# Performance work log

Hardware: AMD Instinct MI355X
Metric: run time of the kernel (lower is better)

## Reference

```python
import jax, jax.numpy as jnp
import numpy as np
from jax import lax

NEG = -1e30  # log-space 'zero' that stays finite for stable grads


def _logadd3(a, b, c):
    m = jnp.maximum(jnp.maximum(a, b), c)
    return m + jnp.log(jnp.exp(a - m) + jnp.exp(b - m) + jnp.exp(c - m))


def _logadd2(a, b):
    m = jnp.maximum(a, b)
    return m + jnp.log(jnp.exp(a - m) + jnp.exp(b - m))


def setup_inputs() -> dict:
    key = jax.random.key(0)
    k1, k2, k3 = jax.random.split(key, 3)
    B, T, V, L = 64, 2000, 512, 200
    logits = jax.random.normal(k1, (B, T, V), dtype=jnp.float32)
    # keep input lengths well above 2*L+1 so all paths are feasible
    input_lengths = (T - jax.random.randint(k2, (B,), 0, 256)).astype(jnp.int32)
    targets = jax.random.randint(k3, (B, L), 0, V, dtype=jnp.int32)  # 0 == pad == blank
    return {"logits": logits, "input_lengths": input_lengths, "targets": targets}


def ctc_loss_sum(logits, input_lengths, targets):
    B, T, V = logits.shape
    L = targets.shape[1]
    S = 2 * L + 1

    lp = jax.nn.log_softmax(logits, axis=-1)  # [B,T,V]

    # compact nonzero targets per row (masked_select equivalent, fixed shape)
    mask = targets != 0
    tlen = mask.sum(-1)  # [B] target_lengths
    pos = jnp.where(mask, jnp.cumsum(mask, axis=1) - 1, L)
    compact = jnp.zeros_like(targets).at[jnp.arange(B)[:, None], pos].set(targets, mode="drop")

    # extended label sequence: blank, y1, blank, y2, ..., blank  -> [B,S]
    s_idx = jnp.arange(S)
    lab_idx = jnp.clip((s_idx - 1) // 2, 0, L - 1)
    ext = jnp.where(s_idx % 2 == 1, compact[:, lab_idx], 0)  # [B,S]

    # skip transition s-2 -> s allowed iff label at s is non-blank and differs from s-2
    ext_m2 = jnp.pad(ext, ((0, 0), (2, 0)))[:, :S]
    skip_ok = (ext != 0) & (ext != ext_m2) & (s_idx >= 2)  # [B,S]

    lpT = jnp.transpose(lp, (1, 0, 2))  # [T,B,V], scan over time

    # init: alpha_0[0]=lp(blank), alpha_0[1]=lp(y1)
    lp0_ext = jnp.take_along_axis(lpT[0], ext[:, :2], axis=1)  # [B,2]
    alpha0 = jnp.full((B, S), NEG, dtype=lp.dtype).at[:, :2].set(lp0_ext)

    def step(alpha, inp):
        lp_t, t = inp
        a1 = jnp.pad(alpha, ((0, 0), (1, 0)), constant_values=NEG)[:, :S]
        a2 = jnp.pad(alpha, ((0, 0), (2, 0)), constant_values=NEG)[:, :S]
        a2 = jnp.where(skip_ok, a2, NEG)
        lp_e = jnp.take_along_axis(lp_t, ext, axis=1)  # [B,S]
        new = _logadd3(alpha, a1, a2) + lp_e
        active = (t < input_lengths)[:, None]
        return jnp.where(active, new, alpha), None

    alphaT, _ = lax.scan(step, alpha0, (lpT[1:], jnp.arange(1, T)))

    # read out at final blank (2*tlen) and final label (2*tlen-1)
    e1 = (2 * tlen)[:, None]
    e2 = (2 * tlen - 1)
    a1 = jnp.take_along_axis(alphaT, e1, axis=1)[:, 0]
    a2 = jnp.where(e2 >= 0,
                   jnp.take_along_axis(alphaT, jnp.clip(e2, 0)[:, None], axis=1)[:, 0],
                   NEG)
    ll = _logadd2(a1, a2)  # [B] log p(targets | logits)
    return -jnp.sum(ll)


def reference(logits, input_lengths, targets):
    return ctc_loss_sum(logits, input_lengths, targets)
```

## Files before the change

### kernel.cpp

```cpp
#include <hip/hip_runtime.h>

#define B_ 64
#define T_ 2000
#define V_ 512
#define L_ 200
#define CPR 7


__device__ __forceinline__ float dpp_shr1_f(float x) {
  return __int_as_float(__builtin_amdgcn_update_dpp(0, __float_as_int(x), 0x138, 0xf, 0xf, true));
}
__device__ __forceinline__ int dpp_shr1_i(int x) {
  return __builtin_amdgcn_update_dpp(0, x, 0x138, 0xf, 0xf, true);
}
__device__ __forceinline__ float dpp_shl1_f(float x) {
  return __int_as_float(__builtin_amdgcn_update_dpp(0, __float_as_int(x), 0x130, 0xf, 0xf, true));
}
__device__ __forceinline__ int dpp_shl1_i(int x) {
  return __builtin_amdgcn_update_dpp(0, x, 0x130, 0xf, 0xf, true);
}
#define DPPADD(v, ctrl, rmask)                                                              \
  v += __int_as_float(__builtin_amdgcn_update_dpp(0, __float_as_int(v), ctrl, rmask, 0xf, true));

__global__ void kz(float* __restrict__ out) { out[0] = 0.0f; }

__global__ __launch_bounds__(512, 1) void ctc_fused(const float* __restrict__ logits,
                                                    const int* __restrict__ lens,
                                                    const int* __restrict__ targets,
                                                    float* __restrict__ AF,
                                                    int* __restrict__ EF,
                                                    float* __restrict__ DD,
                                                    int* __restrict__ EB) {
  const int bx = blockIdx.x;
  const int b = bx >> 1;
  const int dirb = bx & 1;
  const int wid = threadIdx.x >> 6;
  const int lane = threadIdx.x & 63;

  __shared__ __align__(16) float ring[2][CPR][8][256];
  __shared__ __align__(16) float ringbl[2][CPR][8];
  __shared__ __align__(16) float scr[CPR][2][512];
  __shared__ int cmp[256];
  __shared__ int tl_s;

  if (wid == 0) {
    cmp[lane] = 0; cmp[64 + lane] = 0; cmp[128 + lane] = 0; cmp[192 + lane] = 0;
    int base = 0;
#pragma unroll
    for (int cc = 0; cc < 4; ++cc) {
      const int l = cc * 64 + lane;
      const int v = (l < L_) ? targets[b * L_ + l] : 0;
      const unsigned long long mk = __ballot(v != 0);
      const int pos = base + __popcll(mk & ((1ull << lane) - 1ull));
      if (v != 0) cmp[pos] = v;
      base += __popcll(mk);
    }
    if (lane == 0) tl_s = base;
  }
  __syncthreads();

  const int len = lens[b];
  const int nfull = len >> 3;
  const int rem = len & 7;
  const int nch = nfull + (rem ? 1 : 0);
  const int Cf = nch >> 1;
  const int Ntot = dirb ? (nch - Cf) : Cf;
  const int R = (Ntot + CPR - 1) / CPR;
  const int4 c4 = *(const int4*)(&cmp[4 * lane]);

  const int l0 = 4 * lane;
  const bool v0 = l0 + 0 < L_, v1 = l0 + 1 < L_, v2 = l0 + 2 < L_, v3 = l0 + 3 < L_;

  float a0 = 0.f, a1 = 0.f, a2 = 0.f, a3 = 0.f, a4 = 0.f, a5 = 0.f, a6 = 0.f, a7 = 0.f;
  int E = 0;
  float fac = 1.0f;
  float m0 = 0.f, m1 = 0.f, m2 = 0.f, m3 = 0.f, m0n = 0.f;
  float4 LQ0[8], LQ1[8];
  float4 BLa0, BLb0, BLa1, BLb1;

  if (wid == CPR) {
    const int cm1 = __shfl_up(c4.w, 1);
    m0 = (lane > 0 && c4.x != 0 && c4.x != cm1) ? 1.0f : 0.0f;
    m1 = (c4.y != 0 && c4.y != c4.x) ? 1.0f : 0.0f;
    m2 = (c4.z != 0 && c4.z != c4.y) ? 1.0f : 0.0f;
    m3 = (c4.w != 0 && c4.w != c4.z) ? 1.0f : 0.0f;
    m0n = dpp_shl1_f(m0);
    if (!dirb) {
      if (lane == 0) a0 = 1.0f;
    } else {
      const int st = 2 * tl_s;
      if (lane == (st >> 3)) {
        const int e = st & 7;
        a0 = (e == 0) ? 1.0f : 0.0f; a1 = (e == 1) ? 1.0f : 0.0f;
        a2 = (e == 2) ? 1.0f : 0.0f; a3 = (e == 3) ? 1.0f : 0.0f;
        a4 = (e == 4) ? 1.0f : 0.0f; a5 = (e == 5) ? 1.0f : 0.0f;
        a6 = (e == 6) ? 1.0f : 0.0f; a7 = (e == 7) ? 1.0f : 0.0f;
      }
    }
    __builtin_amdgcn_s_setprio(1);
  }

  auto produce = [&](int c, int buf) {
    const float* rowp = logits + (size_t)b * (T_ * V_) + (size_t)c * (8 * V_);
    float4 X[16];
#pragma unroll
    for (int r = 0; r < 8; ++r) {
      X[2 * r] = *(const float4*)(rowp + r * V_ + 4 * lane);
      X[2 * r + 1] = *(const float4*)(rowp + r * V_ + 256 + 4 * lane);
    }
#pragma unroll
    for (int r = 0; r < 8; ++r) {
      const float4 xe = X[2 * r], xo = X[2 * r + 1];
      const float e0 = __expf(xe.x), e1 = __expf(xe.y), e2 = __expf(xe.z), e3 = __expf(xe.w);
      const float e4 = __expf(xo.x), e5 = __expf(xo.y), e6 = __expf(xo.z), e7 = __expf(xo.w);
      float s = ((e0 + e1) + (e2 + e3)) + ((e4 + e5) + (e6 + e7));
      DPPADD(s, 0x111, 0xf); DPPADD(s, 0x112, 0xf); DPPADD(s, 0x114, 0xf);
      DPPADD(s, 0x118, 0xf); DPPADD(s, 0x142, 0xa); DPPADD(s, 0x143, 0xc);
      const float sum = __int_as_float(__builtin_amdgcn_readlane(__float_as_int(s), 63));
      const float inv = 32.0f / sum;
      float* sc = &scr[wid][r & 1][0];
      *(float4*)(sc + 4 * lane) = make_float4(e0, e1, e2, e3);
      *(float4*)(sc + 256 + 4 * lane) = make_float4(e4, e5, e6, e7);
      asm volatile("s_waitcnt lgkmcnt(0)" ::: "memory");
      float4 h;
      h.x = v0 ? sc[c4.x] * inv : 0.0f;
      h.y = v1 ? sc[c4.y] * inv : 0.0f;
      h.z = v2 ? sc[c4.z] * inv : 0.0f;
      h.w = v3 ? sc[c4.w] * inv : 0.0f;
      *(float4*)(&ring[buf][wid][r][4 * lane]) = h;
      if (lane == 0) ringbl[buf][wid][r] = e0 * inv;
    }
  };

#define LDCHUNK(S, BUF, K)                                                   \
  {                                                                          \
    const int bf_ = (BUF), kk_ = (K);                                        \
    _Pragma("unroll") for (int u = 0; u < 8; ++u)                            \
        LQ##S[u] = *(const float4*)(&ring[bf_][kk_][u][4 * lane]);           \
    BLa##S = *(const float4*)(&ringbl[bf_][kk_][0]);                         \
    BLb##S = *(const float4*)(&ringbl[bf_][kk_][4]);                         \
  }

#define STEP8F(S)                                                            \
  {                                                                          \
    const float blv_[8] = {BLa##S.x, BLa##S.y, BLa##S.z, BLa##S.w,           \
                           BLb##S.x, BLb##S.y, BLb##S.z, BLb##S.w};          \
    _Pragma("unroll") for (int u = 0; u < 8; ++u) {                          \
      const float4 hq = LQ##S[u];                                            \
      const float pbv = blv_[u];                                             \
      const float s1 = dpp_shr1_f(a7) * fac;                 \
      float n0 = (a0 + s1) * pbv;                                            \
      float n1 = fmaf(m0, s1, a0 + a1) * hq.x;                               \
      float n2 = (a2 + a1) * pbv;                                            \
      float n3 = fmaf(m1, a1, a2 + a3) * hq.y;                               \
      float n4 = (a4 + a3) * pbv;                                            \
      float n5 = fmaf(m2, a3, a4 + a5) * hq.z;                               \
      float n6 = (a6 + a5) * pbv;                                            \
      float n7 = fmaf(m3, a5, a6 + a7) * hq.w;                               \
      a0 = n0; a1 = n1; a2 = n2; a3 = n3;                                    \
      a4 = n4; a5 = n5; a6 = n6; a7 = n7;                                    \
    }                                                                        \
  }

#define STEP8B(S, UHI)                                                       \
  {                                                                          \
    const float blv_[8] = {BLa##S.x, BLa##S.y, BLa##S.z, BLa##S.w,           \
                           BLb##S.x, BLb##S.y, BLb##S.z, BLb##S.w};          \
    _Pragma("unroll") for (int u = 7; u >= 0; --u) {                         \
      if (u <= (UHI)) {                                                      \
        const float4 hq = LQ##S[u];                                          \
        const float pbv = blv_[u];                                           \
        const float sa = dpp_shl1_f(a0) * fac;              \
        const float sb = dpp_shl1_f(a1) * fac;                               \
        float n0 = (a0 + a1) * pbv;                                          \
        float n1 = fmaf(m1, a3, a1 + a2) * hq.x;                             \
        float n2 = (a2 + a3) * pbv;                                          \
        float n3 = fmaf(m2, a5, a3 + a4) * hq.y;                             \
        float n4 = (a4 + a5) * pbv;                                          \
        float n5 = fmaf(m3, a7, a5 + a6) * hq.z;                             \
        float n6 = (a6 + a7) * pbv;                                          \
        float n7 = fmaf(m0n, sb, a7 + sa) * hq.w;                            \
        a0 = n0; a1 = n1; a2 = n2; a3 = n3;                                  \
        a4 = n4; a5 = n5; a6 = n6; a7 = n7;                                  \
      }                                                                      \
    }                                                                        \
  }

#define RENORM_COMMON                                                        \
    const float mx = fmaxf(fmaxf(fmaxf(a0, a1), fmaxf(a2, a3)),              \
                           fmaxf(fmaxf(a4, a5), fmaxf(a6, a7)));             \
    const bool dead = (mx == 0.0f);                                          \
    int e_ = (int)((__float_as_uint(mx) >> 23) & 0xff) - 127;                \
    if (dead) e_ = 0;                                                        \
    const float sc_ = __int_as_float((unsigned)(127 - e_) << 23);            \
    a0 *= sc_; a1 *= sc_; a2 *= sc_; a3 *= sc_;                              \
    a4 *= sc_; a5 *= sc_; a6 *= sc_; a7 *= sc_;                              \
    const int En_ = E + e_;

#define RENORMF                                                              \
  {                                                                          \
    RENORM_COMMON                                                            \
    const int EnP_ = dpp_shr1_i(En_);                                        \
    E = dead ? EnP_ : En_;                                                   \
    const int Ep_ = dpp_shr1_i(E);                                           \
    const int d_ = Ep_ - E;                                                  \
    int dc_ = d_ < -126 ? -126 : (d_ > 126 ? 126 : d_);                      \
    fac = (d_ < -126) ? 0.0f : __int_as_float((unsigned)(dc_ + 127) << 23);  \
  }

#define RENORMB                                                              \
  {                                                                          \
    RENORM_COMMON                                                            \
    const int EnP_ = dpp_shl1_i(En_);                                        \
    E = dead ? EnP_ : En_;                                                   \
    const int Ep_ = dpp_shl1_i(E);                                           \
    const int d_ = Ep_ - E;                                                  \
    int dc_ = d_ < -126 ? -126 : (d_ > 126 ? 126 : d_);                      \
    fac = (d_ < -126) ? 0.0f : __int_as_float((unsigned)(dc_ + 127) << 23);  \
  }

  if (wid < CPR) {
    const int j = wid;
    if (j < Ntot) produce(dirb ? (nch - 1 - j) : j, 0);
  }
  __syncthreads();

  for (int r = 0; r < R; ++r) {
    if (wid < CPR) {
      const int j = (r + 1) * CPR + wid;
      if (r + 1 < R && j < Ntot) produce(dirb ? (nch - 1 - j) : j, (r + 1) & 1);
    } else {
      int kn = Ntot - r * CPR;
      if (kn > CPR) kn = CPR;
      LDCHUNK(0, r & 1, 0);
      if (!dirb) {
        for (int k = 0; k < kn; ++k) {
          if (k & 1) {
            if (k + 1 < kn) LDCHUNK(0, r & 1, k + 1);
            STEP8F(1);
          } else {
            if (k + 1 < kn) LDCHUNK(1, r & 1, k + 1);
            STEP8F(0);
          }
          RENORMF;
        }
      } else {
        for (int k = 0; k < kn; ++k) {
          const int uh = (r == 0 && k == 0 && rem) ? (rem - 1) : 7;
          if (k & 1) {
            if (k + 1 < kn) LDCHUNK(0, r & 1, k + 1);
            STEP8B(1, uh);
          } else {
            if (k + 1 < kn) LDCHUNK(1, r & 1, k + 1);
            STEP8B(0, uh);
          }
          RENORMB;
        }
      }
    }
    __syncthreads();
  }

  if (wid == CPR) {
    if (!dirb) {
      *(float4*)(AF + b * 512 + lane * 8) = make_float4(a0, a1, a2, a3);
      *(float4*)(AF + b * 512 + lane * 8 + 4) = make_float4(a4, a5, a6, a7);
      EF[b * 64 + lane] = E;
    } else {
      const float sa = dpp_shl1_f(a0) * fac;
      const float sb = dpp_shl1_f(a1) * fac;
      const float d0 = a0 + a1;
      const float d1 = fmaf(m1, a3, a1 + a2);
      const float d2 = a2 + a3;
      const float d3 = fmaf(m2, a5, a3 + a4);
      const float d4 = a4 + a5;
      const float d5 = fmaf(m3, a7, a5 + a6);
      const float d6 = a6 + a7;
      const float d7 = fmaf(m0n, sb, a7 + sa);
      *(float4*)(DD + b * 512 + lane * 8) = make_float4(d0, d1, d2, d3);
      *(float4*)(DD + b * 512 + lane * 8 + 4) = make_float4(d4, d5, d6, d7);
      EB[b * 64 + lane] = E;
    }
  }
#undef LDCHUNK
#undef STEP8F
#undef STEP8B
#undef RENORM_COMMON
#undef RENORMF
#undef RENORMB
}

__global__ __launch_bounds__(64) void kcomb(const int* __restrict__ lens,
                                            const float* __restrict__ AF,
                                            const int* __restrict__ EF,
                                            const float* __restrict__ DD,
                                            const int* __restrict__ EB,
                                            float* __restrict__ out) {
  const int b = blockIdx.x;
  const int lane = threadIdx.x;
  const float4 f0 = *(const float4*)(AF + b * 512 + lane * 8);
  const float4 f1 = *(const float4*)(AF + b * 512 + lane * 8 + 4);
  const float4 g0 = *(const float4*)(DD + b * 512 + lane * 8);
  const float4 g1 = *(const float4*)(DD + b * 512 + lane * 8 + 4);
  const float dot = ((f0.x * g0.x + f0.y * g0.y) + (f0.z * g0.z + f0.w * g0.w)) +
                    ((f1.x * g1.x + f1.y * g1.y) + (f1.z * g1.z + f1.w * g1.w));
  const int Es = EF[b * 64 + lane] + EB[b * 64 + lane];
  const bool z = (dot == 0.0f);
  int Ek = z ? (-(1 << 28)) : Es;
#pragma unroll
  for (int off = 32; off; off >>= 1) {
    const int o = __shfl_xor(Ek, off);
    Ek = o > Ek ? o : Ek;
  }
  float v = z ? 0.0f : ldexpf(dot, Es - Ek);
#pragma unroll
  for (int off = 32; off; off >>= 1) v += __shfl_xor(v, off);
  if (lane == 0) {
    const float ll = __logf(v) + (float)Ek * 0.69314718056f - (float)lens[b] * 3.46573590280f;
    atomicAdd(out, -ll);
  }
}

extern "C" void kernel_launch(void* const* d_in, const int* in_sizes, int n_in,
                              void* d_out, int out_size, void* d_ws, size_t ws_size,
                              hipStream_t stream) {
  const float* logits = (const float*)d_in[0];
  const int* input_lengths = (const int*)d_in[1];
  const int* targets = (const int*)d_in[2];
  float* out = (float*)d_out;
  float* AF = (float*)d_ws;
  int* EF = (int*)(AF + B_ * 512);
  float* DD = (float*)(EF + B_ * 64);
  int* EB = (int*)(DD + B_ * 512);
  (void)in_sizes; (void)n_in; (void)out_size; (void)ws_size;

  kz<<<1, 1, 0, stream>>>(out);
  ctc_fused<<<2 * B_, 512, 0, stream>>>(logits, input_lengths, targets, AF, EF, DD, EB);
  kcomb<<<B_, 64, 0, stream>>>(input_lengths, AF, EF, DD, EB, out);
}
```

Baseline: 396.1 us.

## Split CTC into producer blocks and flag-polling recurrence consumer blocks

Replaces the per-batch 512-thread block, where 7 producer waves fed one recurrence wave through an LDS ring, with a grid of independent 64-thread producer blocks. Each producer block computes the softmax-gathered label probabilities for one 8-frame chunk, stores them to global memory as fp16, and raises a per-chunk flag. 128 consumer blocks run the forward/backward recurrences, polling those flags and prefetching four chunks ahead. The aim is to spread softmax work across the whole GPU instead of capping it at 7 waves per sequence. In exchange it relies on the consumer blocks being scheduled before or alongside the producers, since low-numbered consumers spin-wait and could deadlock otherwise. It also reduces precision to fp16 for label probabilities and replaces the atomic final sum with a single-block reduction.

```diff
diff --git a/kernel.cpp b/kernel.cpp
--- a/kernel.cpp
+++ b/kernel.cpp
@@ -4,8 +4,12 @@
 #define T_ 2000
 #define V_ 512
 #define L_ 200
-#define CPR 7
-
+#define NCONS 128
+#define NPRODB (B_ * 250)
+
+
+typedef _Float16 half4 __attribute__((ext_vector_type(4)));
+union H4U { unsigned long long u; half4 h; float2 f2; };
 
 __device__ __forceinline__ float dpp_shr1_f(float x) {
   return __int_as_float(__builtin_amdgcn_update_dpp(0, __float_as_int(x), 0x138, 0xf, 0xf, true));
@@ -22,85 +26,50 @@
 #define DPPADD(v, ctrl, rmask)                                                              \
   v += __int_as_float(__builtin_amdgcn_update_dpp(0, __float_as_int(v), ctrl, rmask, 0xf, true));
 
-__global__ void kz(float* __restrict__ out) { out[0] = 0.0f; }
-
-__global__ __launch_bounds__(512, 1) void ctc_fused(const float* __restrict__ logits,
-                                                    const int* __restrict__ lens,
-                                                    const int* __restrict__ targets,
-                                                    float* __restrict__ AF,
-                                                    int* __restrict__ EF,
-                                                    float* __restrict__ DD,
-                                                    int* __restrict__ EB) {
-  const int bx = blockIdx.x;
-  const int b = bx >> 1;
-  const int dirb = bx & 1;
-  const int wid = threadIdx.x >> 6;
-  const int lane = threadIdx.x & 63;
-
-  __shared__ __align__(16) float ring[2][CPR][8][256];
-  __shared__ __align__(16) float ringbl[2][CPR][8];
-  __shared__ __align__(16) float scr[CPR][2][512];
+__global__ __launch_bounds__(64) void kflags(int* __restrict__ flags) {
+  const int base = blockIdx.x * 256 + threadIdx.x;
+  flags[base] = 0; flags[base + 64] = 0; flags[base + 128] = 0; flags[base + 192] = 0;
+}
+
+__global__ __launch_bounds__(64, 8) void ctc_split(
+    const float* __restrict__ logits, const int* __restrict__ lens,
+    const int* __restrict__ targets, unsigned long long* __restrict__ cull,
+    unsigned long long* __restrict__ bull, int* __restrict__ flags,
+    float* __restrict__ AF, int* __restrict__ EF,
+    float* __restrict__ DD, int* __restrict__ EB) {
+  const int lane = threadIdx.x;
   __shared__ int cmp[256];
-  __shared__ int tl_s;
-
-  if (wid == 0) {
-    cmp[lane] = 0; cmp[64 + lane] = 0; cmp[128 + lane] = 0; cmp[192 + lane] = 0;
-    int base = 0;
-#pragma unroll
-    for (int cc = 0; cc < 4; ++cc) {
-      const int l = cc * 64 + lane;
-      const int v = (l < L_) ? targets[b * L_ + l] : 0;
-      const unsigned long long mk = __ballot(v != 0);
-      const int pos = base + __popcll(mk & ((1ull << lane) - 1ull));
-      if (v != 0) cmp[pos] = v;
-      base += __popcll(mk);
-    }
-    if (lane == 0) tl_s = base;
-  }
-  __syncthreads();
-
-  const int len = lens[b];
-  const int nfull = len >> 3;
-  const int rem = len & 7;
-  const int nch = nfull + (rem ? 1 : 0);
-  const int Cf = nch >> 1;
-  const int Ntot = dirb ? (nch - Cf) : Cf;
-  const int R = (Ntot + CPR - 1) / CPR;
-  const int4 c4 = *(const int4*)(&cmp[4 * lane]);
-
-  const int l0 = 4 * lane;
-  const bool v0 = l0 + 0 < L_, v1 = l0 + 1 < L_, v2 = l0 + 2 < L_, v3 = l0 + 3 < L_;
-
-  float a0 = 0.f, a1 = 0.f, a2 = 0.f, a3 = 0.f, a4 = 0.f, a5 = 0.f, a6 = 0.f, a7 = 0.f;
-  int E = 0;
-  float fac = 1.0f;
-  float m0 = 0.f, m1 = 0.f, m2 = 0.f, m3 = 0.f, m0n = 0.f;
-  float4 LQ0[8], LQ1[8];
-  float4 BLa0, BLb0, BLa1, BLb1;
-
-  if (wid == CPR) {
-    const int cm1 = __shfl_up(c4.w, 1);
-    m0 = (lane > 0 && c4.x != 0 && c4.x != cm1) ? 1.0f : 0.0f;
-    m1 = (c4.y != 0 && c4.y != c4.x) ? 1.0f : 0.0f;
-    m2 = (c4.z != 0 && c4.z != c4.y) ? 1.0f : 0.0f;
-    m3 = (c4.w != 0 && c4.w != c4.z) ? 1.0f : 0.0f;
-    m0n = dpp_shl1_f(m0);
-    if (!dirb) {
-      if (lane == 0) a0 = 1.0f;
-    } else {
-      const int st = 2 * tl_s;
-      if (lane == (st >> 3)) {
-        const int e = st & 7;
-        a0 = (e == 0) ? 1.0f : 0.0f; a1 = (e == 1) ? 1.0f : 0.0f;
-        a2 = (e == 2) ? 1.0f : 0.0f; a3 = (e == 3) ? 1.0f : 0.0f;
-        a4 = (e == 4) ? 1.0f : 0.0f; a5 = (e == 5) ? 1.0f : 0.0f;
-        a6 = (e == 6) ? 1.0f : 0.0f; a7 = (e == 7) ? 1.0f : 0.0f;
-      }
-    }
-    __builtin_amdgcn_s_setprio(1);
-  }
-
-  auto produce = [&](int c, int buf) {
+  __shared__ __align__(16) float scr[2][512];
+
+#define COMPACT(BB)                                                          \
+  int base = 0;                                                              \
+  {                                                                          \
+    cmp[lane] = 0; cmp[64 + lane] = 0; cmp[128 + lane] = 0; cmp[192 + lane] = 0; \
+    _Pragma("unroll") for (int cc = 0; cc < 4; ++cc) {                       \
+      const int l = cc * 64 + lane;                                          \
+      const int v = (l < L_) ? targets[(BB) * L_ + l] : 0;                   \
+      const unsigned long long mk = __ballot(v != 0);                        \
+      const int pos = base + __popcll(mk & ((1ull << lane) - 1ull));         \
+      if (v != 0) cmp[pos] = v;                                              \
+      base += __popcll(mk);                                                  \
+    }                                                                        \
+    asm volatile("s_waitcnt lgkmcnt(0)" ::: "memory");                       \
+  }
+
+  if ((int)blockIdx.x >= NCONS) {
+    const int g = blockIdx.x - NCONS;
+    const int b = g & 63;
+    const int j = g >> 6;
+    const int len = lens[b];
+    const int nch = (len + 7) >> 3;
+    if (j >= nch) return;
+    const int c = (j & 1) ? (nch - 1 - (j >> 1)) : (j >> 1);
+
+    COMPACT(b);
+    const int4 c4 = *(const int4*)(&cmp[4 * lane]);
+    const int l0 = 4 * lane;
+    const bool v0 = l0 + 0 < L_, v1 = l0 + 1 < L_, v2 = l0 + 2 < L_, v3 = l0 + 3 < L_;
+
     const float* rowp = logits + (size_t)b * (T_ * V_) + (size_t)c * (8 * V_);
     float4 X[16];
 #pragma unroll
@@ -108,6 +77,7 @@
       X[2 * r] = *(const float4*)(rowp + r * V_ + 4 * lane);
       X[2 * r + 1] = *(const float4*)(rowp + r * V_ + 256 + 4 * lane);
     }
+    const size_t obase = ((size_t)(b * T_ + c * 8)) * 64 + lane;
 #pragma unroll
     for (int r = 0; r < 8; ++r) {
       const float4 xe = X[2 * r], xo = X[2 * r + 1];
@@ -118,27 +88,91 @@
       DPPADD(s, 0x118, 0xf); DPPADD(s, 0x142, 0xa); DPPADD(s, 0x143, 0xc);
       const float sum = __int_as_float(__builtin_amdgcn_readlane(__float_as_int(s), 63));
       const float inv = 32.0f / sum;
-      float* sc = &scr[wid][r & 1][0];
+      float* sc = &scr[r & 1][0];
       *(float4*)(sc + 4 * lane) = make_float4(e0, e1, e2, e3);
       *(float4*)(sc + 256 + 4 * lane) = make_float4(e4, e5, e6, e7);
       asm volatile("s_waitcnt lgkmcnt(0)" ::: "memory");
-      float4 h;
-      h.x = v0 ? sc[c4.x] * inv : 0.0f;
-      h.y = v1 ? sc[c4.y] * inv : 0.0f;
-      h.z = v2 ? sc[c4.z] * inv : 0.0f;
-      h.w = v3 ? sc[c4.w] * inv : 0.0f;
-      *(float4*)(&ring[buf][wid][r][4 * lane]) = h;
-      if (lane == 0) ringbl[buf][wid][r] = e0 * inv;
-    }
-  };
-
-#define LDCHUNK(S, BUF, K)                                                   \
-  {                                                                          \
-    const int bf_ = (BUF), kk_ = (K);                                        \
+      H4U p;
+      p.h.x = (_Float16)(v0 ? sc[c4.x] * inv : 0.0f);
+      p.h.y = (_Float16)(v1 ? sc[c4.y] * inv : 0.0f);
+      p.h.z = (_Float16)(v2 ? sc[c4.z] * inv : 0.0f);
+      p.h.w = (_Float16)(v3 ? sc[c4.w] * inv : 0.0f);
+      __hip_atomic_store(cull + obase + (size_t)r * 64, p.u, __ATOMIC_RELAXED,
+                         __HIP_MEMORY_SCOPE_AGENT);
+      if (lane == 0) {
+        unsigned* b32 = (unsigned*)bull;
+        __hip_atomic_store(b32 + b * 2048 + c * 8 + r, __float_as_uint(e0 * inv),
+                           __ATOMIC_RELAXED, __HIP_MEMORY_SCOPE_AGENT);
+      }
+    }
+    asm volatile("s_waitcnt vmcnt(0)" ::: "memory");
+    if (lane == 0)
+      __hip_atomic_store(flags + b * 256 + c, 1, __ATOMIC_RELAXED, __HIP_MEMORY_SCOPE_AGENT);
+    return;
+  }
+
+  const int b = blockIdx.x >> 1;
+  const int dirb = blockIdx.x & 1;
+  const int len = lens[b];
+  const int rem = len & 7;
+  const int nch = (len + 7) >> 3;
+  const int Cf = nch >> 1;
+  const int Ntot = dirb ? (nch - Cf) : Cf;
+
+  COMPACT(b);
+  const int tl = base;
+  const int4 c4 = *(const int4*)(&cmp[4 * lane]);
+
+  const int cm1 = __shfl_up(c4.w, 1);
+  const float m0 = (lane > 0 && c4.x != 0 && c4.x != cm1) ? 1.0f : 0.0f;
+  const float m1 = (c4.y != 0 && c4.y != c4.x) ? 1.0f : 0.0f;
+  const float m2 = (c4.z != 0 && c4.z != c4.y) ? 1.0f : 0.0f;
+  const float m3 = (c4.w != 0 && c4.w != c4.z) ? 1.0f : 0.0f;
+  const float m0n = dpp_shl1_f(m0);
+
+  float a0 = 0.f, a1 = 0.f, a2 = 0.f, a3 = 0.f, a4 = 0.f, a5 = 0.f, a6 = 0.f, a7 = 0.f;
+  int E = 0;
+  float fac = 1.0f;
+  if (!dirb) {
+    if (lane == 0) a0 = 1.0f;
+  } else {
+    const int st = 2 * tl;
+    if (lane == (st >> 3)) {
+      const int e = st & 7;
+      a0 = (e == 0) ? 1.0f : 0.0f; a1 = (e == 1) ? 1.0f : 0.0f;
+      a2 = (e == 2) ? 1.0f : 0.0f; a3 = (e == 3) ? 1.0f : 0.0f;
+      a4 = (e == 4) ? 1.0f : 0.0f; a5 = (e == 5) ? 1.0f : 0.0f;
+      a6 = (e == 6) ? 1.0f : 0.0f; a7 = (e == 7) ? 1.0f : 0.0f;
+    }
+  }
+  __builtin_amdgcn_s_setprio(1);
+
+  unsigned long long LB0[8], LB1[8], LB2[8], LB3[8];
+  float4 BLa0, BLb0, BLa1, BLb1, BLa2, BLb2, BLa3, BLb3;
+
+#define POLL(CIDX)                                                           \
+  {                                                                          \
+    int* fp_ = flags + b * 256 + (CIDX);                                     \
+    while (__hip_atomic_load(fp_, __ATOMIC_RELAXED, __HIP_MEMORY_SCOPE_AGENT) == 0) \
+      __builtin_amdgcn_s_sleep(2);                                           \
+    asm volatile("" ::: "memory");                                           \
+  }
+
+#define LOADC(S, CIDX)                                                       \
+  {                                                                          \
+    const int c_ = (CIDX);                                                   \
+    const size_t base_ = ((size_t)(b * T_ + c_ * 8)) * 64 + lane;            \
     _Pragma("unroll") for (int u = 0; u < 8; ++u)                            \
-        LQ##S[u] = *(const float4*)(&ring[bf_][kk_][u][4 * lane]);           \
-    BLa##S = *(const float4*)(&ringbl[bf_][kk_][0]);                         \
-    BLb##S = *(const float4*)(&ringbl[bf_][kk_][4]);                         \
+        LB##S[u] = __hip_atomic_load(cull + base_ + (size_t)u * 64,          \
+                                     __ATOMIC_RELAXED, __HIP_MEMORY_SCOPE_AGENT); \
+    const size_t bb_ = (size_t)b * 1024 + (size_t)c_ * 4;                    \
+    H4U t0_, t1_, t2_, t3_;                                                  \
+    t0_.u = __hip_atomic_load(bull + bb_ + 0, __ATOMIC_RELAXED, __HIP_MEMORY_SCOPE_AGENT); \
+    t1_.u = __hip_atomic_load(bull + bb_ + 1, __ATOMIC_RELAXED, __HIP_MEMORY_SCOPE_AGENT); \
+    t2_.u = __hip_atomic_load(bull + bb_ + 2, __ATOMIC_RELAXED, __HIP_MEMORY_SCOPE_AGENT); \
+    t3_.u = __hip_atomic_load(bull + bb_ + 3, __ATOMIC_RELAXED, __HIP_MEMORY_SCOPE_AGENT); \
+    BLa##S = make_float4(t0_.f2.x, t0_.f2.y, t1_.f2.x, t1_.f2.y);            \
+    BLb##S = make_float4(t2_.f2.x, t2_.f2.y, t3_.f2.x, t3_.f2.y);            \
   }
 
 #define STEP8F(S)                                                            \
@@ -146,17 +180,19 @@
     const float blv_[8] = {BLa##S.x, BLa##S.y, BLa##S.z, BLa##S.w,           \
                            BLb##S.x, BLb##S.y, BLb##S.z, BLb##S.w};          \
     _Pragma("unroll") for (int u = 0; u < 8; ++u) {                          \
-      const float4 hq = LQ##S[u];                                            \
+      H4U q_; q_.u = LB##S[u];                                               \
+      const float qx = (float)q_.h.x, qy = (float)q_.h.y;                    \
+      const float qz = (float)q_.h.z, qw = (float)q_.h.w;                    \
       const float pbv = blv_[u];                                             \
       const float s1 = dpp_shr1_f(a7) * fac;                 \
       float n0 = (a0 + s1) * pbv;                                            \
-      float n1 = fmaf(m0, s1, a0 + a1) * hq.x;                               \
+      float n1 = fmaf(m0, s1, a0 + a1) * qx;                                 \
       float n2 = (a2 + a1) * pbv;                                            \
-      float n3 = fmaf(m1, a1, a2 + a3) * hq.y;                               \
+      float n3 = fmaf(m1, a1, a2 + a3) * qy;                                 \
       float n4 = (a4 + a3) * pbv;                                            \
-      float n5 = fmaf(m2, a3, a4 + a5) * hq.z;                               \
+      float n5 = fmaf(m2, a3, a4 + a5) * qz;                                 \
       float n6 = (a6 + a5) * pbv;                                            \
-      float n7 = fmaf(m3, a5, a6 + a7) * hq.w;                               \
+      float n7 = fmaf(m3, a5, a6 + a7) * qw;                                 \
       a0 = n0; a1 = n1; a2 = n2; a3 = n3;                                    \
       a4 = n4; a5 = n5; a6 = n6; a7 = n7;                                    \
     }                                                                        \
@@ -168,18 +204,20 @@
                            BLb##S.x, BLb##S.y, BLb##S.z, BLb##S.w};          \
     _Pragma("unroll") for (int u = 7; u >= 0; --u) {                         \
       if (u <= (UHI)) {                                                      \
-        const float4 hq = LQ##S[u];                                          \
+        H4U q_; q_.u = LB##S[u];                                             \
+        const float qx = (float)q_.h.x, qy = (float)q_.h.y;                  \
+        const float qz = (float)q_.h.z, qw = (float)q_.h.w;                  \
         const float pbv = blv_[u];                                           \
         const float sa = dpp_shl1_f(a0) * fac;              \
         const float sb = dpp_shl1_f(a1) * fac;                               \
         float n0 = (a0 + a1) * pbv;                                          \
-        float n1 = fmaf(m1, a3, a1 + a2) * hq.x;                             \
+        float n1 = fmaf(m1, a3, a1 + a2) * qx;                               \
         float n2 = (a2 + a3) * pbv;                                          \
-        float n3 = fmaf(m2, a5, a3 + a4) * hq.y;                             \
+        float n3 = fmaf(m2, a5, a3 + a4) * qy;                               \
         float n4 = (a4 + a5) * pbv;                                          \
-        float n5 = fmaf(m3, a7, a5 + a6) * hq.z;                             \
+        float n5 = fmaf(m3, a7, a5 + a6) * qz;                               \
         float n6 = (a6 + a7) * pbv;                                          \
-        float n7 = fmaf(m0n, sb, a7 + sa) * hq.w;                            \
+        float n7 = fmaf(m0n, sb, a7 + sa) * qw;                              \
         a0 = n0; a1 = n1; a2 = n2; a3 = n3;                                  \
         a4 = n4; a5 = n5; a6 = n6; a7 = n7;                                  \
       }                                                                      \
@@ -219,105 +257,100 @@
     fac = (d_ < -126) ? 0.0f : __int_as_float((unsigned)(dc_ + 127) << 23);  \
   }
 
-  if (wid < CPR) {
-    const int j = wid;
-    if (j < Ntot) produce(dirb ? (nch - 1 - j) : j, 0);
-  }
-  __syncthreads();
-
-  for (int r = 0; r < R; ++r) {
-    if (wid < CPR) {
-      const int j = (r + 1) * CPR + wid;
-      if (r + 1 < R && j < Ntot) produce(dirb ? (nch - 1 - j) : j, (r + 1) & 1);
-    } else {
-      int kn = Ntot - r * CPR;
-      if (kn > CPR) kn = CPR;
-      LDCHUNK(0, r & 1, 0);
-      if (!dirb) {
-        for (int k = 0; k < kn; ++k) {
-          if (k & 1) {
-            if (k + 1 < kn) LDCHUNK(0, r & 1, k + 1);
-            STEP8F(1);
-          } else {
-            if (k + 1 < kn) LDCHUNK(1, r & 1, k + 1);
-            STEP8F(0);
-          }
-          RENORMF;
-        }
-      } else {
-        for (int k = 0; k < kn; ++k) {
-          const int uh = (r == 0 && k == 0 && rem) ? (rem - 1) : 7;
-          if (k & 1) {
-            if (k + 1 < kn) LDCHUNK(0, r & 1, k + 1);
-            STEP8B(1, uh);
-          } else {
-            if (k + 1 < kn) LDCHUNK(1, r & 1, k + 1);
-            STEP8B(0, uh);
-          }
-          RENORMB;
-        }
+  if (!dirb) {
+    POLL(0); LOADC(0, 0); POLL(1); LOADC(1, 1);
+    POLL(2); LOADC(2, 2); POLL(3); LOADC(3, 3);
+    for (int i = 0; i < Ntot; ++i) {
+      const int nx = i + 4;
+      const bool pf = nx < Ntot;
+      switch (i & 3) {
+        case 0: STEP8F(0); RENORMF; if (pf) { POLL(nx); LOADC(0, nx); } break;
+        case 1: STEP8F(1); RENORMF; if (pf) { POLL(nx); LOADC(1, nx); } break;
+        case 2: STEP8F(2); RENORMF; if (pf) { POLL(nx); LOADC(2, nx); } break;
+        default: STEP8F(3); RENORMF; if (pf) { POLL(nx); LOADC(3, nx); } break;
       }
     }
-    __syncthreads();
-  }
-
-  if (wid == CPR) {
-    if (!dirb) {
-      *(float4*)(AF + b * 512 + lane * 8) = make_float4(a0, a1, a2, a3);
-      *(float4*)(AF + b * 512 + lane * 8 + 4) = make_float4(a4, a5, a6, a7);
-      EF[b * 64 + lane] = E;
-    } else {
-      const float sa = dpp_shl1_f(a0) * fac;
-      const float sb = dpp_shl1_f(a1) * fac;
-      const float d0 = a0 + a1;
-      const float d1 = fmaf(m1, a3, a1 + a2);
-      const float d2 = a2 + a3;
-      const float d3 = fmaf(m2, a5, a3 + a4);
-      const float d4 = a4 + a5;
-      const float d5 = fmaf(m3, a7, a5 + a6);
-      const float d6 = a6 + a7;
-      const float d7 = fmaf(m0n, sb, a7 + sa);
-      *(float4*)(DD + b * 512 + lane * 8) = make_float4(d0, d1, d2, d3);
-      *(float4*)(DD + b * 512 + lane * 8 + 4) = make_float4(d4, d5, d6, d7);
-      EB[b * 64 + lane] = E;
-    }
-  }
-#undef LDCHUNK
+    *(float4*)(AF + b * 512 + lane * 8) = make_float4(a0, a1, a2, a3);
+    *(float4*)(AF + b * 512 + lane * 8 + 4) = make_float4(a4, a5, a6, a7);
+    EF[b * 64 + lane] = E;
+  } else {
+    POLL(nch - 1); LOADC(0, nch - 1); POLL(nch - 2); LOADC(1, nch - 2);
+    POLL(nch - 3); LOADC(2, nch - 3); POLL(nch - 4); LOADC(3, nch - 4);
+    for (int i = 0; i < Ntot; ++i) {
+      const int nx = i + 4;
+      const bool pf = nx < Ntot;
+      const int cx = nch - 1 - nx;
+      const int uh = (i == 0 && rem) ? (rem - 1) : 7;
+      switch (i & 3) {
+        case 0: STEP8B(0, uh); RENORMB; if (pf) { POLL(cx); LOADC(0, cx); } break;
+        case 1: STEP8B(1, uh); RENORMB; if (pf) { POLL(cx); LOADC(1, cx); } break;
+        case 2: STEP8B(2, uh); RENORMB; if (pf) { POLL(cx); LOADC(2, cx); } break;
+        default: STEP8B(3, uh); RENORMB; if (pf) { POLL(cx); LOADC(3, cx); } break;
+      }
+    }
+    const float sa = dpp_shl1_f(a0) * fac;
+    const float sb = dpp_shl1_f(a1) * fac;
+    const float d0 = a0 + a1;
+    const float d1 = fmaf(m1, a3, a1 + a2);
+    const float d2 = a2 + a3;
+    const float d3 = fmaf(m2, a5, a3 + a4);
+    const float d4 = a4 + a5;
+    const float d5 = fmaf(m3, a7, a5 + a6);
+    const float d6 = a6 + a7;
+    const float d7 = fmaf(m0n, sb, a7 + sa);
+    *(float4*)(DD + b * 512 + lane * 8) = make_float4(d0, d1, d2, d3);
+    *(float4*)(DD + b * 512 + lane * 8 + 4) = make_float4(d4, d5, d6, d7);
+    EB[b * 64 + lane] = E;
+  }
+#undef POLL
+#undef LOADC
 #undef STEP8F
 #undef STEP8B
 #undef RENORM_COMMON
 #undef RENORMF
 #undef RENORMB
-}
-
-__global__ __launch_bounds__(64) void kcomb(const int* __restrict__ lens,
-                                            const float* __restrict__ AF,
-                                            const int* __restrict__ EF,
-                                            const float* __restrict__ DD,
-                                            const int* __restrict__ EB,
-                                            float* __restrict__ out) {
-  const int b = blockIdx.x;
-  const int lane = threadIdx.x;
-  const float4 f0 = *(const float4*)(AF + b * 512 + lane * 8);
-  const float4 f1 = *(const float4*)(AF + b * 512 + lane * 8 + 4);
-  const float4 g0 = *(const float4*)(DD + b * 512 + lane * 8);
-  const float4 g1 = *(const float4*)(DD + b * 512 + lane * 8 + 4);
-  const float dot = ((f0.x * g0.x + f0.y * g0.y) + (f0.z * g0.z + f0.w * g0.w)) +
-                    ((f1.x * g1.x + f1.y * g1.y) + (f1.z * g1.z + f1.w * g1.w));
-  const int Es = EF[b * 64 + lane] + EB[b * 64 + lane];
-  const bool z = (dot == 0.0f);
-  int Ek = z ? (-(1 << 28)) : Es;
-#pragma unroll
-  for (int off = 32; off; off >>= 1) {
-    const int o = __shfl_xor(Ek, off);
-    Ek = o > Ek ? o : Ek;
-  }
-  float v = z ? 0.0f : ldexpf(dot, Es - Ek);
-#pragma unroll
-  for (int off = 32; off; off >>= 1) v += __shfl_xor(v, off);
-  if (lane == 0) {
+#undef COMPACT
+}
+
+__global__ __launch_bounds__(512) void kcomb(const int* __restrict__ lens,
+                                             const float* __restrict__ AF,
+                                             const int* __restrict__ EF,
+                                             const float* __restrict__ DD,
+                                             const int* __restrict__ EB,
+                                             float* __restrict__ out) {
+  const int wid = threadIdx.x >> 6;
+  const int lane = threadIdx.x & 63;
+  __shared__ float part[8];
+  float acc = 0.0f;
+#pragma unroll
+  for (int q = 0; q < 8; ++q) {
+    const int b = wid * 8 + q;
+    const float4 f0 = *(const float4*)(AF + b * 512 + lane * 8);
+    const float4 f1 = *(const float4*)(AF + b * 512 + lane * 8 + 4);
+    const float4 g0 = *(const float4*)(DD + b * 512 + lane * 8);
+    const float4 g1 = *(const float4*)(DD + b * 512 + lane * 8 + 4);
+    const float dot = ((f0.x * g0.x + f0.y * g0.y) + (f0.z * g0.z + f0.w * g0.w)) +
+                      ((f1.x * g1.x + f1.y * g1.y) + (f1.z * g1.z + f1.w * g1.w));
+    const int Es = EF[b * 64 + lane] + EB[b * 64 + lane];
+    const bool z = (dot == 0.0f);
+    int Ek = z ? (-(1 << 28)) : Es;
+#pragma unroll
+    for (int off = 32; off; off >>= 1) {
+      const int o = __shfl_xor(Ek, off);
+      Ek = o > Ek ? o : Ek;
+    }
+    float v = z ? 0.0f : ldexpf(dot, Es - Ek);
+#pragma unroll
+    for (int off = 32; off; off >>= 1) v += __shfl_xor(v, off);
     const float ll = __logf(v) + (float)Ek * 0.69314718056f - (float)lens[b] * 3.46573590280f;
-    atomicAdd(out, -ll);
+    acc -= ll;
+  }
+  if (lane == 0) part[wid] = acc;
+  __syncthreads();
+  if (threadIdx.x == 0) {
+    float s = ((part[0] + part[1]) + (part[2] + part[3])) +
+              ((part[4] + part[5]) + (part[6] + part[7]));
+    out[0] = s;
   }
 }
 
@@ -328,13 +361,17 @@
   const int* input_lengths = (const int*)d_in[1];
   const int* targets = (const int*)d_in[2];
   float* out = (float*)d_out;
-  float* AF = (float*)d_ws;
-  int* EF = (int*)(AF + B_ * 512);
-  float* DD = (float*)(EF + B_ * 64);
-  int* EB = (int*)(DD + B_ * 512);
+  unsigned long long* cull = (unsigned long long*)d_ws;
+  unsigned long long* bull = (unsigned long long*)((char*)d_ws + 65536000);
+  int* flags = (int*)((char*)d_ws + 66060288);
+  float* AF = (float*)((char*)d_ws + 66125824);
+  int* EF = (int*)((char*)d_ws + 66256896);
+  float* DD = (float*)((char*)d_ws + 66273280);
+  int* EB = (int*)((char*)d_ws + 66404352);
   (void)in_sizes; (void)n_in; (void)out_size; (void)ws_size;
 
-  kz<<<1, 1, 0, stream>>>(out);
-  ctc_fused<<<2 * B_, 512, 0, stream>>>(logits, input_lengths, targets, AF, EF, DD, EB);
-  kcomb<<<B_, 64, 0, stream>>>(input_lengths, AF, EF, DD, EB, out);
-}
+  kflags<<<B_, 64, 0, stream>>>(flags);
+  ctc_split<<<NCONS + NPRODB, 64, 0, stream>>>(logits, input_lengths, targets,
+                                               cull, bull, flags, AF, EF, DD, EB);
+  kcomb<<<1, 512, 0, stream>>>(input_lengths, AF, EF, DD, EB, out);
+}
```

Result: slower. 933.8 us (+135.8%).
